# Optimization experiments

Measured on AMD Instinct MI355X. Metric: run time of the kernel, lower is better.

The kernel has to match this reference:

```python
import jax, jax.numpy as jnp
import numpy as np

B, D, E, H, F, V = 65536, 8, 16, 80, 9, 100000
IN = E * (F + 1)  # 160


def setup_inputs() -> dict:
    key = jax.random.key(0)
    ks = jax.random.split(key, 14)
    pid = jax.random.randint(ks[0], (B,), 0, D + 1)            # 0 = padding, 1..D = domains
    feats = jax.random.randint(ks[1], (B, F), 0, V)
    emb_pid = (jax.random.normal(ks[2], (D + 1, E), jnp.float32) * 0.1).at[0].set(0.0)
    emb_feats = (jax.random.normal(ks[3], (F, V + 1, E), jnp.float32) * 0.1).at[:, 0, :].set(0.0)
    shared_w1 = jax.random.normal(ks[4], (IN, H), jnp.float32) * 0.1
    dom_w1 = jax.random.normal(ks[5], (D, IN, H), jnp.float32) * 0.1
    shared_b1 = jax.random.normal(ks[6], (H,), jnp.float32) * 0.1
    dom_b1 = jax.random.normal(ks[7], (D, H), jnp.float32) * 0.1
    shared_w2 = jax.random.normal(ks[8], (H,), jnp.float32) * 0.1
    dom_w2 = jax.random.normal(ks[9], (D, H), jnp.float32) * 0.1
    shared_b2 = jax.random.normal(ks[10], (), jnp.float32) * 0.1
    dom_b2 = jax.random.normal(ks[11], (D,), jnp.float32) * 0.1
    dl_w = jax.random.normal(ks[12], (E,), jnp.float32) * 0.1
    dl_b = jax.random.normal(ks[13], (), jnp.float32) * 0.1
    return {"pid": pid, "feats": feats, "emb_pid": emb_pid, "emb_feats": emb_feats,
            "shared_w1": shared_w1, "dom_w1": dom_w1, "shared_b1": shared_b1, "dom_b1": dom_b1,
            "shared_w2": shared_w2, "dom_w2": dom_w2, "shared_b2": shared_b2, "dom_b2": dom_b2,
            "dl_w": dl_w, "dl_b": dl_b}


def reference(pid, feats, emb_pid, emb_feats, shared_w1, dom_w1, shared_b1, dom_b1,
              shared_w2, dom_w2, shared_b2, dom_b2, dl_w, dl_b):
    # embedding lookup + relu (dropout is identity at inference)
    e_pid = jax.nn.relu(emb_pid[pid])                          # (B, E)
    e_f = jax.nn.relu(emb_feats[jnp.arange(F), feats])         # (B, F, E)
    out = jnp.concatenate([e_pid, e_f.reshape(B, F * E)], axis=-1)  # (B, IN)
    # star-merge: elementwise product of shared and per-domain kernels, additive biases
    W1 = shared_w1[None] * dom_w1                              # (D, IN, H)
    b1 = shared_b1[None] + dom_b1                              # (D, H)
    h = jax.nn.relu(jnp.einsum('bi,dih->dbh', out, W1) + b1[:, None, :])  # (D, B, H)
    W2 = shared_w2[None] * dom_w2                              # (D, H)
    b2 = shared_b2 + dom_b2                                    # (D,)
    l = jnp.einsum('dbh,dh->db', h, W2) + b2[:, None]          # (D, B)
    # scatter-combine: each sample takes its own domain's logit (0 for padding pid)
    sel = pid[None, :] == (jnp.arange(D) + 1)[:, None]         # (D, B)
    logits = jnp.sum(jnp.where(sel, l, 0.0), axis=0)           # (B,)
    domain_logits = e_pid @ dl_w + dl_b                        # (B,)
    return logits + domain_logits
```

## Files before the change

### kernel.cpp

```cpp
#include <hip/hip_runtime.h>

#define NB 65536
#define ND 8
#define NE 16
#define NH 80
#define NF 9
#define NV 100000
#define NIN 160
#define WND 512

typedef __attribute__((ext_vector_type(8))) short short8;
typedef __attribute__((ext_vector_type(4))) float float4v;

#define WS_W1BF   0
#define WS_B1F    51200
#define WS_W2F    51840
#define WS_B2F    52480

__device__ inline unsigned short f2bf(float x) {
  unsigned int u = __float_as_uint(x);
  return (unsigned short)((u + 0x7fffu + ((u >> 16) & 1u)) >> 16);
}

__global__ void k_fuse(const float* __restrict__ sw1, const float* __restrict__ dw1,
                       const float* __restrict__ sb1, const float* __restrict__ db1,
                       const float* __restrict__ sw2, const float* __restrict__ dw2,
                       const float* __restrict__ sb2, const float* __restrict__ db2,
                       unsigned int* __restrict__ w1bf, float* __restrict__ wsf) {
  int t = blockIdx.x * 256 + threadIdx.x;
  if (t < ND * NH * (NIN / 2)) {
    int d = t / (NH * (NIN / 2));
    int r = t % (NH * (NIN / 2));
    int n = r / (NIN / 2);
    int k0 = (r % (NIN / 2)) * 2;
    float a = sw1[k0 * NH + n] * dw1[d * NIN * NH + k0 * NH + n];
    float b = sw1[(k0 + 1) * NH + n] * dw1[d * NIN * NH + (k0 + 1) * NH + n];
    w1bf[t] = (unsigned)f2bf(a) | ((unsigned)f2bf(b) << 16);
  }
  if (t < ND * NH) {
    wsf[WS_B1F + t] = sb1[t % NH] + db1[t];
    wsf[WS_W2F + t] = sw2[t % NH] * dw2[t];
  }
  if (t < ND) wsf[WS_B2F + t] = sb2[0] + db2[t];
}

__global__ __launch_bounds__(256) void k_main(
    const int* __restrict__ pid, const int* __restrict__ feats,
    const float* __restrict__ emb_pid, const float* __restrict__ emb_feats,
    const float* __restrict__ dl_w, const float* __restrict__ dl_b,
    const unsigned int* __restrict__ w1bf, const float* __restrict__ wsf,
    float* __restrict__ out) {
  const int d = blockIdx.x & 7;
  const int wnd = blockIdx.x >> 3;
  const int t = threadIdx.x, wave = t >> 6, lane = t & 63;

  __shared__ unsigned short sA[64][168];
  __shared__ unsigned short sB[80][168];
  __shared__ int sid[WND];
  __shared__ int cnt[2][4];

  const int b0 = wnd * WND + t;
  const int b1 = b0 + 256;
  const int p0 = pid[b0];
  const int p1 = pid[b1];

  const unsigned int* __restrict__ wb = w1bf + d * (NH * (NIN / 2));
  for (int i = t; i < NH * (NIN / 2); i += 256) {
    int n = i / (NIN / 2), kp = i % (NIN / 2);
    ((unsigned int*)&sB[n][0])[kp] = wb[i];
  }

  const float dlb = dl_b[0];
  if (d == 0) {
    if (p0 == 0) out[b0] = dlb;
    if (p1 == 0) out[b1] = dlb;
  }

  unsigned long long m0 = __ballot(p0 == d + 1);
  unsigned long long m1 = __ballot(p1 == d + 1);
  if (lane == 0) { cnt[0][wave] = (int)__popcll(m0); cnt[1][wave] = (int)__popcll(m1); }
  const int r0 = (int)__popcll(m0 & ((1ull << lane) - 1ull));
  const int r1 = (int)__popcll(m1 & ((1ull << lane) - 1ull));

  float dlacc = dlb;
  unsigned int ep[8];
  {
    const float* __restrict__ row = emb_pid + (d + 1) * NE;
#pragma unroll
    for (int i = 0; i < NE; i += 2) {
      float x0 = fmaxf(row[i], 0.f), x1 = fmaxf(row[i + 1], 0.f);
      dlacc = fmaf(x0, dl_w[i], dlacc);
      dlacc = fmaf(x1, dl_w[i + 1], dlacc);
      ep[i >> 1] = (unsigned)f2bf(x0) | ((unsigned)f2bf(x1) << 16);
    }
  }
  const float b2 = wsf[WS_B2F + d];
  float b1l[5], w2l[5];
#pragma unroll
  for (int nt = 0; nt < 5; ++nt) {
    b1l[nt] = wsf[WS_B1F + d * NH + nt * 16 + (lane & 15)];
    w2l[nt] = wsf[WS_W2F + d * NH + nt * 16 + (lane & 15)];
  }

  __syncthreads();
  int base0 = 0, base1 = 0;
#pragma unroll
  for (int w = 0; w < 4; ++w) {
    if (w < wave) { base0 += cnt[0][w]; base1 += cnt[1][w]; }
  }
  const int tot0 = cnt[0][0] + cnt[0][1] + cnt[0][2] + cnt[0][3];
  const int c = tot0 + cnt[1][0] + cnt[1][1] + cnt[1][2] + cnt[1][3];
  if (p0 == d + 1) sid[base0 + r0] = b0;
  if (p1 == d + 1) sid[tot0 + base1 + r1] = b1;
  __syncthreads();

  for (int g0 = 0; g0 < c; g0 += 64) {
    const int s = t >> 2, q = t & 3;
    const int ss = g0 + s;
    const int bb = sid[ss < c ? ss : 0];
    int idx[NF];
#pragma unroll
    for (int f = 0; f < NF; ++f) idx[f] = feats[bb * NF + f];
    float4 vv[NF];
#pragma unroll
    for (int f = 0; f < NF; ++f)
      vv[f] = ((const float4*)(emb_feats + ((size_t)f * (NV + 1) + (size_t)idx[f]) * NE))[q];
    if (q < 2) {
      unsigned int* dst = (unsigned int*)&sA[s][0];
#pragma unroll
      for (int j = 0; j < 4; ++j) dst[q * 4 + j] = ep[q * 4 + j];
    }
#pragma unroll
    for (int f = 0; f < NF; ++f) {
      unsigned int pk0 = (unsigned)f2bf(fmaxf(vv[f].x, 0.f)) |
                         ((unsigned)f2bf(fmaxf(vv[f].y, 0.f)) << 16);
      unsigned int pk1 = (unsigned)f2bf(fmaxf(vv[f].z, 0.f)) |
                         ((unsigned)f2bf(fmaxf(vv[f].w, 0.f)) << 16);
      unsigned int* dst = (unsigned int*)&sA[s][16 + f * 16];
      dst[q * 2] = pk0;
      dst[q * 2 + 1] = pk1;
    }
    __syncthreads();

    float4v acc[5];
#pragma unroll
    for (int nt = 0; nt < 5; ++nt)
      acc[nt] = (float4v){b1l[nt], b1l[nt], b1l[nt], b1l[nt]};
    const int arow = wave * 16 + (lane & 15);
    const int koff = (lane >> 4) * 8;
#pragma unroll
    for (int ks = 0; ks < 5; ++ks) {
      short8 af = *(const short8*)&sA[arow][ks * 32 + koff];
#pragma unroll
      for (int nt = 0; nt < 5; ++nt) {
        short8 bf = *(const short8*)&sB[nt * 16 + (lane & 15)][ks * 32 + koff];
        acc[nt] = __builtin_amdgcn_mfma_f32_16x16x32_bf16(af, bf, acc[nt], 0, 0, 0);
      }
    }

    float pr[4];
#pragma unroll
    for (int r = 0; r < 4; ++r) {
      float a2 = 0.f;
#pragma unroll
      for (int nt = 0; nt < 5; ++nt) a2 = fmaf(fmaxf(acc[nt][r], 0.f), w2l[nt], a2);
      pr[r] = a2;
    }
#pragma unroll
    for (int r = 0; r < 4; ++r) {
      pr[r] += __shfl_xor(pr[r], 1);
      pr[r] += __shfl_xor(pr[r], 2);
      pr[r] += __shfl_xor(pr[r], 4);
      pr[r] += __shfl_xor(pr[r], 8);
    }
    if ((lane & 15) == 0) {
      int srow = wave * 16 + (lane >> 4) * 4;
#pragma unroll
      for (int r = 0; r < 4; ++r) {
        int kk = g0 + srow + r;
        if (kk < c) out[sid[kk]] = pr[r] + b2 + dlacc;
      }
    }
    __syncthreads();
  }
}

extern "C" void kernel_launch(void* const* d_in, const int* in_sizes, int n_in,
                              void* d_out, int out_size, void* d_ws, size_t ws_size,
                              hipStream_t stream) {
  const int*   pid      = (const int*)d_in[0];
  const int*   feats    = (const int*)d_in[1];
  const float* emb_pid  = (const float*)d_in[2];
  const float* emb_f    = (const float*)d_in[3];
  const float* sw1      = (const float*)d_in[4];
  const float* dw1      = (const float*)d_in[5];
  const float* sb1      = (const float*)d_in[6];
  const float* db1      = (const float*)d_in[7];
  const float* sw2      = (const float*)d_in[8];
  const float* dw2      = (const float*)d_in[9];
  const float* sb2      = (const float*)d_in[10];
  const float* db2      = (const float*)d_in[11];
  const float* dl_w     = (const float*)d_in[12];
  const float* dl_b     = (const float*)d_in[13];
  float* out = (float*)d_out;
  float* wsf = (float*)d_ws;
  unsigned int* w1bf = (unsigned int*)d_ws;

  k_fuse<<<(ND * NH * (NIN / 2) + 255) / 256, 256, 0, stream>>>(
      sw1, dw1, sb1, db1, sw2, dw2, sb2, db2, w1bf, wsf);
  k_main<<<(NB / WND) * ND, 256, 0, stream>>>(pid, feats, emb_pid, emb_f,
                                              dl_w, dl_b, w1bf, wsf, out);
}
```

Baseline: 29.75 us.

## Fold weight-merge prep into main kernel, double block size, pre-swizzle B fragments

Removes the separate k_fuse launch: each block now computes the star-merged W1 (shared*domain product, bf16) directly into a fragment-ordered LDS layout, along with its own b1/w2/b2. Blocks grow to 512 threads covering 1024 samples, so the kernel processes 128 rows per MFMA pass. Conversions use the packed bf16 intrinsic, and the trailing barrier is skipped on the last iteration. This trades a second kernel launch for redundant per-block weight merging (512 blocks each recompute 12.8K products) and larger LDS usage that may reduce occupancy.

```diff
diff --git a/kernel.cpp b/kernel.cpp
--- a/kernel.cpp
+++ b/kernel.cpp
@@ -1,4 +1,5 @@
 #include <hip/hip_runtime.h>
+#include <hip/hip_bf16.h>
 
 #define NB 65536
 #define ND 8
@@ -7,81 +8,52 @@
 #define NF 9
 #define NV 100000
 #define NIN 160
-#define WND 512
+#define WND 1024
+#define NWND (NB / WND)
 
 typedef __attribute__((ext_vector_type(8))) short short8;
 typedef __attribute__((ext_vector_type(4))) float float4v;
-
-#define WS_W1BF   0
-#define WS_B1F    51200
-#define WS_W2F    51840
-#define WS_B2F    52480
 
 __device__ inline unsigned short f2bf(float x) {
   unsigned int u = __float_as_uint(x);
   return (unsigned short)((u + 0x7fffu + ((u >> 16) & 1u)) >> 16);
 }
-
-__global__ void k_fuse(const float* __restrict__ sw1, const float* __restrict__ dw1,
-                       const float* __restrict__ sb1, const float* __restrict__ db1,
-                       const float* __restrict__ sw2, const float* __restrict__ dw2,
-                       const float* __restrict__ sb2, const float* __restrict__ db2,
-                       unsigned int* __restrict__ w1bf, float* __restrict__ wsf) {
-  int t = blockIdx.x * 256 + threadIdx.x;
-  if (t < ND * NH * (NIN / 2)) {
-    int d = t / (NH * (NIN / 2));
-    int r = t % (NH * (NIN / 2));
-    int n = r / (NIN / 2);
-    int k0 = (r % (NIN / 2)) * 2;
-    float a = sw1[k0 * NH + n] * dw1[d * NIN * NH + k0 * NH + n];
-    float b = sw1[(k0 + 1) * NH + n] * dw1[d * NIN * NH + (k0 + 1) * NH + n];
-    w1bf[t] = (unsigned)f2bf(a) | ((unsigned)f2bf(b) << 16);
-  }
-  if (t < ND * NH) {
-    wsf[WS_B1F + t] = sb1[t % NH] + db1[t];
-    wsf[WS_W2F + t] = sw2[t % NH] * dw2[t];
-  }
-  if (t < ND) wsf[WS_B2F + t] = sb2[0] + db2[t];
+__device__ inline unsigned int cvt2(float x, float y) {
+  union { __hip_bfloat162 h; unsigned int u; } cv;
+  cv.h = __float22bfloat162_rn(make_float2(x, y));
+  return cv.u;
 }
 
-__global__ __launch_bounds__(256) void k_main(
+__global__ __launch_bounds__(512, 4) void k_main(
     const int* __restrict__ pid, const int* __restrict__ feats,
     const float* __restrict__ emb_pid, const float* __restrict__ emb_feats,
+    const float* __restrict__ sw1, const float* __restrict__ dw1,
+    const float* __restrict__ sb1, const float* __restrict__ db1,
+    const float* __restrict__ sw2, const float* __restrict__ dw2,
+    const float* __restrict__ sb2, const float* __restrict__ db2,
     const float* __restrict__ dl_w, const float* __restrict__ dl_b,
-    const unsigned int* __restrict__ w1bf, const float* __restrict__ wsf,
     float* __restrict__ out) {
-  const int d = blockIdx.x & 7;
-  const int wnd = blockIdx.x >> 3;
+  const int d = blockIdx.x >> 6;
+  const int wnd = blockIdx.x & 63;
   const int t = threadIdx.x, wave = t >> 6, lane = t & 63;
 
-  __shared__ unsigned short sA[64][168];
-  __shared__ unsigned short sB[80][168];
-  __shared__ int sid[WND];
-  __shared__ int cnt[2][4];
+  __shared__ unsigned short sA[128][168];
+  __shared__ unsigned short sBF[5][5][4][16][8];
+  __shared__ int sOrig[WND];
+  __shared__ int cnt0[8], cnt1[8];
 
   const int b0 = wnd * WND + t;
-  const int b1 = b0 + 256;
+  const int b1 = b0 + 512;
   const int p0 = pid[b0];
   const int p1 = pid[b1];
 
-  const unsigned int* __restrict__ wb = w1bf + d * (NH * (NIN / 2));
-  for (int i = t; i < NH * (NIN / 2); i += 256) {
-    int n = i / (NIN / 2), kp = i % (NIN / 2);
-    ((unsigned int*)&sB[n][0])[kp] = wb[i];
+  for (int i = t; i < NIN * NH; i += 512) {
+    int k = i / NH, n = i % NH;
+    float w = sw1[i] * dw1[d * (NIN * NH) + i];
+    sBF[n >> 4][k >> 5][(k >> 3) & 3][n & 15][k & 7] = f2bf(w);
   }
 
   const float dlb = dl_b[0];
-  if (d == 0) {
-    if (p0 == 0) out[b0] = dlb;
-    if (p1 == 0) out[b1] = dlb;
-  }
-
-  unsigned long long m0 = __ballot(p0 == d + 1);
-  unsigned long long m1 = __ballot(p1 == d + 1);
-  if (lane == 0) { cnt[0][wave] = (int)__popcll(m0); cnt[1][wave] = (int)__popcll(m1); }
-  const int r0 = (int)__popcll(m0 & ((1ull << lane) - 1ull));
-  const int r1 = (int)__popcll(m1 & ((1ull << lane) - 1ull));
-
   float dlacc = dlb;
   unsigned int ep[8];
   {
@@ -91,40 +63,54 @@
       float x0 = fmaxf(row[i], 0.f), x1 = fmaxf(row[i + 1], 0.f);
       dlacc = fmaf(x0, dl_w[i], dlacc);
       dlacc = fmaf(x1, dl_w[i + 1], dlacc);
-      ep[i >> 1] = (unsigned)f2bf(x0) | ((unsigned)f2bf(x1) << 16);
+      ep[i >> 1] = cvt2(x0, x1);
     }
   }
-  const float b2 = wsf[WS_B2F + d];
   float b1l[5], w2l[5];
 #pragma unroll
   for (int nt = 0; nt < 5; ++nt) {
-    b1l[nt] = wsf[WS_B1F + d * NH + nt * 16 + (lane & 15)];
-    w2l[nt] = wsf[WS_W2F + d * NH + nt * 16 + (lane & 15)];
+    int h = nt * 16 + (lane & 15);
+    b1l[nt] = sb1[h] + db1[d * NH + h];
+    w2l[nt] = sw2[h] * dw2[d * NH + h];
+  }
+  const float b2 = sb2[0] + db2[d];
+
+  if (d == 0) {
+    if (p0 == 0) out[b0] = dlb;
+    if (p1 == 0) out[b1] = dlb;
   }
 
+  unsigned long long m0 = __ballot(p0 == d + 1);
+  unsigned long long m1 = __ballot(p1 == d + 1);
+  if (lane == 0) { cnt0[wave] = (int)__popcll(m0); cnt1[wave] = (int)__popcll(m1); }
+  const unsigned long long lt = (1ull << lane) - 1ull;
+  const int r0 = (int)__popcll(m0 & lt);
+  const int r1 = (int)__popcll(m1 & lt);
   __syncthreads();
-  int base0 = 0, base1 = 0;
+  int base0 = 0, tot0 = 0, base1 = 0, tot1 = 0;
 #pragma unroll
-  for (int w = 0; w < 4; ++w) {
-    if (w < wave) { base0 += cnt[0][w]; base1 += cnt[1][w]; }
+  for (int w = 0; w < 8; ++w) {
+    if (w < wave) { base0 += cnt0[w]; base1 += cnt1[w]; }
+    tot0 += cnt0[w]; tot1 += cnt1[w];
   }
-  const int tot0 = cnt[0][0] + cnt[0][1] + cnt[0][2] + cnt[0][3];
-  const int c = tot0 + cnt[1][0] + cnt[1][1] + cnt[1][2] + cnt[1][3];
-  if (p0 == d + 1) sid[base0 + r0] = b0;
-  if (p1 == d + 1) sid[tot0 + base1 + r1] = b1;
+  const int c = tot0 + tot1;
+  if (p0 == d + 1) sOrig[base0 + r0] = b0;
+  if (p1 == d + 1) sOrig[tot0 + base1 + r1] = b1;
   __syncthreads();
 
-  for (int g0 = 0; g0 < c; g0 += 64) {
+  for (int g0 = 0; g0 < c; g0 += 128) {
     const int s = t >> 2, q = t & 3;
-    const int ss = g0 + s;
-    const int bb = sid[ss < c ? ss : 0];
+    int ss = g0 + s; if (ss >= c) ss = c - 1;
+    const int bb = sOrig[ss];
+
     int idx[NF];
 #pragma unroll
     for (int f = 0; f < NF; ++f) idx[f] = feats[bb * NF + f];
     float4 vv[NF];
 #pragma unroll
     for (int f = 0; f < NF; ++f)
-      vv[f] = ((const float4*)(emb_feats + ((size_t)f * (NV + 1) + (size_t)idx[f]) * NE))[q];
+      vv[f] = *(const float4*)(emb_feats +
+                               (size_t)((f * (NV + 1) + idx[f]) * NE + q * 4));
     if (q < 2) {
       unsigned int* dst = (unsigned int*)&sA[s][0];
 #pragma unroll
@@ -132,13 +118,11 @@
     }
 #pragma unroll
     for (int f = 0; f < NF; ++f) {
-      unsigned int pk0 = (unsigned)f2bf(fmaxf(vv[f].x, 0.f)) |
-                         ((unsigned)f2bf(fmaxf(vv[f].y, 0.f)) << 16);
-      unsigned int pk1 = (unsigned)f2bf(fmaxf(vv[f].z, 0.f)) |
-                         ((unsigned)f2bf(fmaxf(vv[f].w, 0.f)) << 16);
+      unsigned int lo = cvt2(fmaxf(vv[f].x, 0.f), fmaxf(vv[f].y, 0.f));
+      unsigned int hi = cvt2(fmaxf(vv[f].z, 0.f), fmaxf(vv[f].w, 0.f));
       unsigned int* dst = (unsigned int*)&sA[s][16 + f * 16];
-      dst[q * 2] = pk0;
-      dst[q * 2 + 1] = pk1;
+      dst[q * 2] = lo;
+      dst[q * 2 + 1] = hi;
     }
     __syncthreads();
 
@@ -153,7 +137,7 @@
       short8 af = *(const short8*)&sA[arow][ks * 32 + koff];
 #pragma unroll
       for (int nt = 0; nt < 5; ++nt) {
-        short8 bf = *(const short8*)&sB[nt * 16 + (lane & 15)][ks * 32 + koff];
+        short8 bf = *(const short8*)&sBF[nt][ks][lane >> 4][lane & 15][0];
         acc[nt] = __builtin_amdgcn_mfma_f32_16x16x32_bf16(af, bf, acc[nt], 0, 0, 0);
       }
     }
@@ -174,14 +158,14 @@
       pr[r] += __shfl_xor(pr[r], 8);
     }
     if ((lane & 15) == 0) {
-      int srow = wave * 16 + (lane >> 4) * 4;
+      int srow2 = wave * 16 + (lane >> 4) * 4;
 #pragma unroll
       for (int r = 0; r < 4; ++r) {
-        int kk = g0 + srow + r;
-        if (kk < c) out[sid[kk]] = pr[r] + b2 + dlacc;
+        int kk = g0 + srow2 + r;
+        if (kk < c) out[sOrig[kk]] = pr[r] + b2 + dlacc;
       }
     }
-    __syncthreads();
+    if (g0 + 128 < c) __syncthreads();
   }
 }
 
@@ -203,11 +187,9 @@
   const float* dl_w     = (const float*)d_in[12];
   const float* dl_b     = (const float*)d_in[13];
   float* out = (float*)d_out;
-  float* wsf = (float*)d_ws;
-  unsigned int* w1bf = (unsigned int*)d_ws;
+  (void)d_ws; (void)ws_size;
 
-  k_fuse<<<(ND * NH * (NIN / 2) + 255) / 256, 256, 0, stream>>>(
-      sw1, dw1, sb1, db1, sw2, dw2, sb2, db2, w1bf, wsf);
-  k_main<<<(NB / WND) * ND, 256, 0, stream>>>(pid, feats, emb_pid, emb_f,
-                                              dl_w, dl_b, w1bf, wsf, out);
+  k_main<<<NWND * ND, 512, 0, stream>>>(pid, feats, emb_pid, emb_f, sw1, dw1,
+                                        sb1, db1, sw2, dw2, sb2, db2, dl_w,
+                                        dl_b, out);
 }
```

Measured after the change: 26.87 us. 9.7% less time.
